# Kernel tuning notes

Measured on AMD Instinct MI355X. Metric: run time of the kernel, lower is better.

Reference implementation:

```python
import jax, jax.numpy as jnp
import numpy as np

INF = 1.0e9
MU = 1e-8
SAFE_THRESHOLD = 0.05
B = 128
N = 512            # NORMALIZED_SIZE
OBS = 8            # observation steps
PARTITIONS = 8
MAX_PARTITIONS = 16
VISION_RADIUS = 2.0
TWO_PI = 2.0 * np.pi


def setup_inputs() -> dict:
    key = jax.random.key(0)
    k1, k2, k3, k4, k5 = jax.random.split(key, 5)
    # segmentation maps in [0, 1]; values <= 0.05 are 'safe' pixels
    seg_maps = jax.random.uniform(k1, (B, N, N), dtype=jnp.float32)
    # paras: W (pixels-per-meter scale) in [2.5, 3.5], b (pixel offset) in [0, 20]
    Wscale = jax.random.uniform(k2, (B, 2), dtype=jnp.float32, minval=2.5, maxval=3.5)
    boffs = jax.random.uniform(k3, (B, 2), dtype=jnp.float32, minval=0.0, maxval=20.0)
    seg_map_paras = jnp.concatenate([Wscale, boffs], axis=-1)  # [B, 4]
    trajectories = 2.0 * jax.random.normal(k4, (B, OBS, 2), dtype=jnp.float32)
    # reference points near the middle of the (meters-space) map
    current_pos = 80.0 + 5.0 * jax.random.normal(k5, (B, 1, 2), dtype=jnp.float32)
    # pixel-center grid (pool_size = 1 -> map_pos_pixel = pixel indices)
    xs, ys = jnp.meshgrid(jnp.arange(N), jnp.arange(N), indexing='ij')
    map_pos_pixel = jnp.stack([xs.reshape(-1), ys.reshape(-1)], axis=-1).astype(jnp.float32)  # [N*N, 2]
    return {
        'seg_maps': seg_maps,
        'seg_map_paras': seg_map_paras,
        'trajectories': trajectories,
        'current_pos': current_pos,
        'map_pos_pixel': map_pos_pixel,
    }


def reference(seg_maps, seg_map_paras, trajectories, current_pos, map_pos_pixel):
    b = seg_maps.shape[0]
    _obs = trajectories + current_pos                        # [B, OBS, 2]
    maps_flat = seg_maps.reshape(b, -1)                      # [B, P]
    safe = maps_flat <= SAFE_THRESHOLD                       # [B, P] bool

    moving_vector = _obs[:, -1, :] - _obs[:, 0, :]           # [B, 2]
    moving_length = jnp.linalg.norm(moving_vector, axis=-1)  # [B]

    Wp = seg_map_paras[:, None, :2]                          # [B, 1, 2]
    bp = seg_map_paras[:, None, 2:4]                         # [B, 1, 2]
    map_pos = (map_pos_pixel[None] - bp) / Wp                # [B, P, 2]

    dvec = map_pos - current_pos                             # [B, P, 2]
    dist = jnp.linalg.norm(dvec, axis=-1)                    # [B, P]
    angles = jnp.arctan2(dvec[..., 0], dvec[..., 1])         # [B, P]
    bin_idx = ((angles % TWO_PI) / (TWO_PI / PARTITIONS)).astype(jnp.int32)  # [B, P]

    equ_dis = (dist + MU) / (maps_flat + MU)                 # [B, P]
    r = (VISION_RADIUS * moving_length)[:, None]             # [B, 1]
    valid = (~safe) & (dist <= r)                            # [B, P]
    d = jnp.where(valid, equ_dis, INF)                       # [B, P]

    # single-pass per-angle-bin min (replaces the per-partition Python loop)
    seg_min = jax.vmap(
        lambda dv, bi: jax.ops.segment_min(dv, bi, num_segments=PARTITIONS)
    )(d, bin_idx)                                            # [B, K]
    min_d = jnp.minimum(seg_min, INF)                        # empty segments -> INF
    obstacle = (min_d < INF).astype(d.dtype)                 # [B, K]

    f_velocity = moving_length[:, None] * obstacle           # [B, K]
    f_min_distance = min_d * obstacle                        # [B, K]
    centers = (TWO_PI * (jnp.arange(PARTITIONS, dtype=d.dtype) + 0.5) / PARTITIONS)
    f_direction = centers[None, :] * obstacle                # [B, K]

    pc = jnp.stack([f_velocity, f_min_distance, f_direction], axis=-1)  # [B, K, 3]
    pc = jnp.pad(pc, ((0, 0), (0, MAX_PARTITIONS - PARTITIONS), (0, 0)))
    return pc
```

## Files before the change

### kernel.cpp

```cpp
#include <hip/hip_runtime.h>
#include <math.h>

#define BATCH 128
#define NN 512
#define PARTS 8
#define INF_F 1000000000.0f
#define MU_F 1e-8f
#define SAFE_T 0.05f
#define TWO_PI_F 6.28318530717958647692f
#define STEP_F 0.78539816339744830962f
#define NT 1024

__global__ __launch_bounds__(NT) void pc_kernel(
    const float* __restrict__ seg_maps,
    const float* __restrict__ paras,
    const float* __restrict__ traj,
    const float* __restrict__ cpos,
    float* __restrict__ out)
{
    const int b   = blockIdx.x;
    const int tid = threadIdx.x;

    const float Wx = paras[b * 4 + 0];
    const float Wy = paras[b * 4 + 1];
    const float bx = paras[b * 4 + 2];
    const float by = paras[b * 4 + 3];
    const float cx = cpos[b * 2 + 0];
    const float cy = cpos[b * 2 + 1];

    const float o0x = traj[b * 16 + 0]  + cx;
    const float o0y = traj[b * 16 + 1]  + cy;
    const float o7x = traj[b * 16 + 14] + cx;
    const float o7y = traj[b * 16 + 15] + cy;
    const float mvx = o7x - o0x;
    const float mvy = o7y - o0y;
    const float ml  = __fsqrt_rn(__fadd_rn(__fmul_rn(mvx, mvx), __fmul_rn(mvy, mvy)));
    const float r   = 2.0f * ml;

    int ilo = (int)floorf(bx + Wx * (cx - r)) - 2;
    int ihi = (int)ceilf (bx + Wx * (cx + r)) + 2;
    int jlo = (int)floorf(by + Wy * (cy - r)) - 2;
    int jhi = (int)ceilf (by + Wy * (cy + r)) + 2;
    ilo = max(ilo, 0); ihi = min(ihi, NN - 1);
    jlo = max(jlo, 0); jhi = min(jhi, NN - 1);

    int h = 0, w = 0;
    if (ilo <= ihi && jlo <= jhi) {
        h = ihi - ilo + 1;
        w = jhi - jlo + 1;
    }

    __shared__ float dxs[NN];
    __shared__ float dys[NN];
    for (int t = tid; t < h; t += NT)
        dxs[t] = __fdiv_rn((float)(ilo + t) - bx, Wx) - cx;
    for (int t = tid; t < w; t += NT)
        dys[t] = __fdiv_rn((float)(jlo + t) - by, Wy) - cy;
    __syncthreads();

    float mind[PARTS];
#pragma unroll
    for (int k = 0; k < PARTS; ++k) mind[k] = INF_F;

    if (h > 0) {
        const float* mb = seg_maps + (size_t)b * NN * NN;
        const int ti = tid >> 6;
        const int tj = tid & 63;

        for (int jj = tj; jj < w; jj += 64) {
            const float dy = dys[jj];
            const int j = jlo + jj;
            for (int ii = ti; ii < h; ii += 16) {
                const float dx = dxs[ii];
                const float m  = mb[(ilo + ii) * NN + j];
                const float s  = __fadd_rn(__fmul_rn(dx, dx), __fmul_rn(dy, dy));
                const float dist = __fsqrt_rn(s);
                if (m > SAFE_T && dist <= r) {
                    const float ang = atan2f(dx, dy);
                    const float am  = (ang < 0.0f) ? (ang + (float)TWO_PI_F) : ang;
                    const int bin   = (int)__fdiv_rn(am, (float)STEP_F);
                    if (bin < PARTS) {
                        const float ed = __fdiv_rn(dist + MU_F, m + MU_F);
                        mind[bin] = fminf(mind[bin], ed);
                    }
                }
            }
        }
    }

    __shared__ float red[16 * PARTS];
    const int lane = tid & 63;
    const int wave = tid >> 6;
#pragma unroll
    for (int k = 0; k < PARTS; ++k) {
        float v = mind[k];
#pragma unroll
        for (int off = 32; off >= 1; off >>= 1)
            v = fminf(v, __shfl_xor(v, off, 64));
        if (lane == 0) red[wave * PARTS + k] = v;
    }
    __syncthreads();

    if (tid < 48) {
        const int k = tid / 3;
        const int c = tid % 3;
        float val = 0.0f;
        if (k < PARTS) {
            float mn = INF_F;
#pragma unroll
            for (int wv = 0; wv < 16; ++wv)
                mn = fminf(mn, red[wv * PARTS + k]);
            if (mn < INF_F) {
                if (c == 0)      val = ml;
                else if (c == 1) val = mn;
                else             val = __fdiv_rn(__fmul_rn((float)TWO_PI_F, (float)k + 0.5f), 8.0f);
            }
        }
        out[b * 48 + k * 3 + c] = val;
    }
}

extern "C" void kernel_launch(void* const* d_in, const int* in_sizes, int n_in,
                              void* d_out, int out_size, void* d_ws, size_t ws_size,
                              hipStream_t stream) {
    const float* seg_maps = (const float*)d_in[0];
    const float* paras    = (const float*)d_in[1];
    const float* traj     = (const float*)d_in[2];
    const float* cpos     = (const float*)d_in[3];

    pc_kernel<<<BATCH, NT, 0, stream>>>(seg_maps, paras, traj, cpos, (float*)d_out);
}
```

Measured before the change: 177.2 us.

## Split per-batch work across 8 blocks of 256 threads with two-pass reduction

The single 1024-thread block per batch is replaced by a grid of BATCH x 8 blocks of 256 threads, each covering an interleaved subset of rows of the bounding box. Per-block minima go to a workspace and a second small kernel reduces them and writes the output. Shared-memory precomputation of dx/dy is dropped in favour of recomputing the divisions inline. The aim is better distribution of work across compute units and higher occupancy, at the cost of an extra launch, redundant divisions, and a workspace round-trip.

```diff
diff --git a/kernel.cpp b/kernel.cpp
--- a/kernel.cpp
+++ b/kernel.cpp
@@ -4,21 +4,22 @@
 #define BATCH 128
 #define NN 512
 #define PARTS 8
+#define YSPLIT 8
 #define INF_F 1000000000.0f
 #define MU_F 1e-8f
 #define SAFE_T 0.05f
 #define TWO_PI_F 6.28318530717958647692f
 #define STEP_F 0.78539816339744830962f
-#define NT 1024
 
-__global__ __launch_bounds__(NT) void pc_kernel(
+__global__ __launch_bounds__(256) void pc_compute(
     const float* __restrict__ seg_maps,
     const float* __restrict__ paras,
     const float* __restrict__ traj,
     const float* __restrict__ cpos,
-    float* __restrict__ out)
+    float* __restrict__ ws)
 {
     const int b   = blockIdx.x;
+    const int y   = blockIdx.y;
     const int tid = threadIdx.x;
 
     const float Wx = paras[b * 4 + 0];
@@ -44,34 +45,24 @@
     ilo = max(ilo, 0); ihi = min(ihi, NN - 1);
     jlo = max(jlo, 0); jhi = min(jhi, NN - 1);
 
-    int h = 0, w = 0;
-    if (ilo <= ihi && jlo <= jhi) {
-        h = ihi - ilo + 1;
-        w = jhi - jlo + 1;
-    }
-
-    __shared__ float dxs[NN];
-    __shared__ float dys[NN];
-    for (int t = tid; t < h; t += NT)
-        dxs[t] = __fdiv_rn((float)(ilo + t) - bx, Wx) - cx;
-    for (int t = tid; t < w; t += NT)
-        dys[t] = __fdiv_rn((float)(jlo + t) - by, Wy) - cy;
-    __syncthreads();
-
     float mind[PARTS];
 #pragma unroll
     for (int k = 0; k < PARTS; ++k) mind[k] = INF_F;
 
-    if (h > 0) {
+    if (ilo <= ihi && jlo <= jhi) {
+        const int h = ihi - ilo + 1;
+        const int w = jhi - jlo + 1;
         const float* mb = seg_maps + (size_t)b * NN * NN;
+
         const int ti = tid >> 6;
         const int tj = tid & 63;
+        const int gw = y * 4 + ti;
 
         for (int jj = tj; jj < w; jj += 64) {
-            const float dy = dys[jj];
+            const float dy = __fdiv_rn((float)(jlo + jj) - by, Wy) - cy;
             const int j = jlo + jj;
-            for (int ii = ti; ii < h; ii += 16) {
-                const float dx = dxs[ii];
+            for (int ii = gw; ii < h; ii += 32) {
+                const float dx = __fdiv_rn((float)(ilo + ii) - bx, Wx) - cx;
                 const float m  = mb[(ilo + ii) * NN + j];
                 const float s  = __fadd_rn(__fmul_rn(dx, dx), __fmul_rn(dy, dy));
                 const float dist = __fsqrt_rn(s);
@@ -88,7 +79,7 @@
         }
     }
 
-    __shared__ float red[16 * PARTS];
+    __shared__ float red[4 * PARTS];
     const int lane = tid & 63;
     const int wave = tid >> 6;
 #pragma unroll
@@ -101,23 +92,51 @@
     }
     __syncthreads();
 
-    if (tid < 48) {
-        const int k = tid / 3;
-        const int c = tid % 3;
-        float val = 0.0f;
-        if (k < PARTS) {
-            float mn = INF_F;
+    if (tid < PARTS) {
+        const float mn = fminf(fminf(red[0 * PARTS + tid], red[1 * PARTS + tid]),
+                               fminf(red[2 * PARTS + tid], red[3 * PARTS + tid]));
+        ws[(b * YSPLIT + y) * PARTS + tid] = mn;
+    }
+}
+
+__global__ __launch_bounds__(256) void pc_finalize(
+    const float* __restrict__ traj,
+    const float* __restrict__ cpos,
+    const float* __restrict__ ws,
+    float* __restrict__ out)
+{
+    const int g = blockIdx.x * 256 + threadIdx.x;
+    if (g >= BATCH * 48) return;
+    const int b   = g / 48;
+    const int rem = g - b * 48;
+    const int k   = rem / 3;
+    const int c   = rem - k * 3;
+
+    float val = 0.0f;
+    if (k < PARTS) {
+        float mn = INF_F;
 #pragma unroll
-            for (int wv = 0; wv < 16; ++wv)
-                mn = fminf(mn, red[wv * PARTS + k]);
-            if (mn < INF_F) {
-                if (c == 0)      val = ml;
-                else if (c == 1) val = mn;
-                else             val = __fdiv_rn(__fmul_rn((float)TWO_PI_F, (float)k + 0.5f), 8.0f);
+        for (int y = 0; y < YSPLIT; ++y)
+            mn = fminf(mn, ws[(b * YSPLIT + y) * PARTS + k]);
+        if (mn < INF_F) {
+            if (c == 0) {
+                const float cx = cpos[b * 2 + 0];
+                const float cy = cpos[b * 2 + 1];
+                const float o0x = traj[b * 16 + 0]  + cx;
+                const float o0y = traj[b * 16 + 1]  + cy;
+                const float o7x = traj[b * 16 + 14] + cx;
+                const float o7y = traj[b * 16 + 15] + cy;
+                const float mvx = o7x - o0x;
+                const float mvy = o7y - o0y;
+                val = __fsqrt_rn(__fadd_rn(__fmul_rn(mvx, mvx), __fmul_rn(mvy, mvy)));
+            } else if (c == 1) {
+                val = mn;
+            } else {
+                val = __fdiv_rn(__fmul_rn((float)TWO_PI_F, (float)k + 0.5f), 8.0f);
             }
         }
-        out[b * 48 + k * 3 + c] = val;
     }
+    out[g] = val;
 }
 
 extern "C" void kernel_launch(void* const* d_in, const int* in_sizes, int n_in,
@@ -128,5 +147,8 @@
     const float* traj     = (const float*)d_in[2];
     const float* cpos     = (const float*)d_in[3];
 
-    pc_kernel<<<BATCH, NT, 0, stream>>>(seg_maps, paras, traj, cpos, (float*)d_out);
+    float* ws = (float*)d_ws;
+
+    pc_compute<<<dim3(BATCH, YSPLIT), 256, 0, stream>>>(seg_maps, paras, traj, cpos, ws);
+    pc_finalize<<<(BATCH * 48 + 255) / 256, 256, 0, stream>>>(traj, cpos, ws, (float*)d_out);
 }
```

Result: no change. 174.0 us (-1.8%).
